# Optimization experiments

Hardware: AMD Instinct MI355X
Metric: run time of the kernel (lower is better)

The kernel has to match this reference:

```python
import jax, jax.numpy as jnp
import numpy as np

GAMMA = 0.9
SCALE_BASE = 512.0


def _xpos(x, downscale=False):
    """XPOS rotary embedding (torchscale variant) applied to x: (B, L, D)."""
    B, L, D = x.shape
    half = D // 2
    # per-channel magnitude base: ((2i) + 0.4*D) / (1.4*D), i over even channels
    scale_vec = (jnp.arange(0, D, 2, dtype=jnp.float32) + 0.4 * D) / (1.4 * D)  # (half,)
    power = jnp.arange(L, dtype=jnp.float32) / SCALE_BASE                        # (L,)
    scale = scale_vec[None, :] ** power[:, None]                                 # (L, half)
    if downscale:
        scale = 1.0 / scale
    # fixed sinusoidal frequencies over `half` dims
    inv_freq = 1.0 / (10000.0 ** (jnp.arange(half, dtype=jnp.float32) / half))   # (half,)
    sinusoid = jnp.arange(L, dtype=jnp.float32)[:, None] * inv_freq[None, :]     # (L, half)
    sin = jnp.repeat(jnp.sin(sinusoid) * scale, 2, axis=-1)                      # (L, D) interleaved dup
    cos = jnp.repeat(jnp.cos(sinusoid) * scale, 2, axis=-1)
    # rotate_every_two: (x0,x1,x2,x3,...) -> (-x1,x0,-x3,x2,...)
    x_even = x[..., 0::2]
    x_odd = x[..., 1::2]
    rot = jnp.stack((-x_odd, x_even), axis=-1).reshape(x.shape)
    return x * cos + rot * sin


def _get_D(seq_len):
    n = jnp.arange(seq_len, dtype=jnp.float32)[:, None]
    m = jnp.arange(seq_len, dtype=jnp.float32)[None, :]
    D = GAMMA ** jnp.abs(n - m)  # non-causal decay, no NaNs since gamma > 0
    return D


def setup_inputs() -> dict:
    key = jax.random.key(0)
    k1, k2, k3, k4 = jax.random.split(key, 4)
    B, L, H, Dh = 8, 2048, 1024, 1024
    X = jax.random.normal(k1, (B, L, H), dtype=jnp.float32)
    W_Q = jax.random.normal(k2, (H, Dh), dtype=jnp.float32) / H
    W_K = jax.random.normal(k3, (H, Dh), dtype=jnp.float32) / H
    W_V = jax.random.normal(k4, (H, Dh), dtype=jnp.float32) / H
    return {"X": X, "W_Q": W_Q, "W_K": W_K, "W_V": W_V}


def reference(X, W_Q, W_K, W_V):
    B, L, H = X.shape
    D = _get_D(L)                       # (L, L)
    Q = _xpos(X @ W_Q)                  # (B, L, Dh)
    K = _xpos(X @ W_K, downscale=True)  # (B, L, Dh)
    V = X @ W_V                         # (B, L, Dv)
    scores = jnp.einsum('bqd,bkd->bqk', Q, K)   # (B, L, L)
    p_attn = jax.nn.softmax(scores, axis=-1)
    p_attn = p_attn * D[None, :, :]              # elementwise decay AFTER softmax
    return jnp.einsum('bqk,bkv->bqv', p_attn, V)
```

## Files before the change

### kernel.cpp

```cpp
#include <hip/hip_runtime.h>
#include <math.h>


#define LDIM 2048
#define HDIM 1024
#define MTOT 16384

typedef unsigned short u16;
typedef unsigned int u32;
typedef __attribute__((ext_vector_type(4))) float f32x4;
typedef __attribute__((ext_vector_type(8))) short s16x8;

#define GLD16(gp, lp) __builtin_amdgcn_global_load_lds( \
    (const __attribute__((address_space(1))) void*)(gp), \
    (__attribute__((address_space(3))) void*)(lp), 16, 0, 0)

__device__ __forceinline__ u16 f2bf(float f) {
    unsigned u = __float_as_uint(f);
    return (u16)((u + 0x7FFFu + ((u >> 16) & 1u)) >> 16);
}

__device__ __forceinline__ void sincos_rev(float ang, float* sn, float* cs) {
    double dr = (double)ang * 0.15915494309189535;
    dr -= __builtin_floor(dr);
    float fr = (float)dr;
    float s_, c_;
    asm("v_sin_f32 %0, %1" : "=v"(s_) : "v"(fr));
    asm("v_cos_f32 %0, %1" : "=v"(c_) : "v"(fr));
    *sn = s_; *cs = c_;
}

__device__ __forceinline__ void gemm256h(const u16* __restrict__ A,
                                         const u16* __restrict__ B,
                                         int lda, int ldb, int K, int m0, int n0,
                                         char* smem, int tid, f32x4 (*acc)[4])
{
    const int wv = tid >> 6, ln = tid & 63;
    const int wm = wv >> 2, wn = wv & 3;
    const int lr = ln & 15, lg = ln >> 4;
    const int srow = tid >> 3;
    const int scol = ((tid & 7) ^ (srow & 7)) * 8;

    const u16* ap[4];
    const u16* bp[4];
#pragma unroll
    for (int r = 0; r < 4; ++r) {
        ap[r] = A + (size_t)(m0 + r * 64 + srow) * lda + scol;
        bp[r] = B + (size_t)(n0 + r * 64 + srow) * ldb + scol;
    }

    int arow[8], brow[4];
#pragma unroll
    for (int fm = 0; fm < 8; ++fm) arow[fm] = (wm * 128 + fm * 16 + lr) * 128;
#pragma unroll
    for (int fn = 0; fn < 4; ++fn) brow[fn] = 32768 + (wn * 64 + fn * 16 + lr) * 128;
    int slotb[2];
#pragma unroll
    for (int kk = 0; kk < 2; ++kk) slotb[kk] = (((kk << 2) | lg) ^ (lr & 7)) << 4;

#define STAGEALL(e_) do { char* d_ = smem + (e_) * 65536 + tid * 16;          \
        _Pragma("unroll") for (int r_ = 0; r_ < 4; ++r_) {                    \
            GLD16(ap[r_], d_ + r_ * 8192);          ap[r_] += 64; }           \
        _Pragma("unroll") for (int r_ = 0; r_ < 4; ++r_) {                    \
            GLD16(bp[r_], d_ + 32768 + r_ * 8192);  bp[r_] += 64; }           \
    } while (0)

#define RD_A(Bb_, mh) do {                                                    \
        _Pragma("unroll") for (int fm_ = 0; fm_ < 4; ++fm_)                   \
            _Pragma("unroll") for (int kk_ = 0; kk_ < 2; ++kk_)               \
                aq[fm_ * 2 + kk_] = *(const s16x8*)((Bb_) +                   \
                    arow[(mh) * 4 + fm_] + slotb[kk_]);                       \
    } while (0)
#define RD_B(Bb_, nh, dst) do {                                               \
        _Pragma("unroll") for (int fn_ = 0; fn_ < 2; ++fn_)                   \
            _Pragma("unroll") for (int kk_ = 0; kk_ < 2; ++kk_)               \
                dst[fn_ * 2 + kk_] = *(const s16x8*)((Bb_) +                  \
                    brow[(nh) * 2 + fn_] + slotb[kk_]);                       \
    } while (0)

#define MFMA16(mh, nh, bq_) do {                                              \
        _Pragma("unroll") for (int fm_ = 0; fm_ < 4; ++fm_)                   \
            _Pragma("unroll") for (int fn_ = 0; fn_ < 2; ++fn_)               \
                _Pragma("unroll") for (int kk_ = 0; kk_ < 2; ++kk_)           \
                    acc[(mh) * 4 + fm_][(nh) * 2 + fn_] =                     \
                        __builtin_amdgcn_mfma_f32_16x16x32_bf16(              \
                            aq[fm_ * 2 + kk_], bq_[fn_ * 2 + kk_],            \
                            acc[(mh) * 4 + fm_][(nh) * 2 + fn_], 0, 0, 0);    \
    } while (0)

    const int nk = K >> 6;

    STAGEALL(0);
    __syncthreads();

    s16x8 aq[8], b0[4], b1[4];

#pragma unroll 1
    for (int t = 0; t < nk; ++t) {
        const int d = t & 1, e = d ^ 1;
        if (t + 1 < nk) STAGEALL(e);
        const char* Bb = smem + d * 65536;
        RD_A(Bb, 0); RD_B(Bb, 0, b0);
        MFMA16(0, 0, b0);
        RD_B(Bb, 1, b1);
        MFMA16(0, 1, b1);
        RD_A(Bb, 1);
        MFMA16(1, 1, b1);
        MFMA16(1, 0, b0);
        __syncthreads();
    }
    __syncthreads();
#undef STAGEALL
#undef RD_A
#undef RD_B
#undef MFMA16
}

__global__ __launch_bounds__(256) void prep_all(
    const float* __restrict__ X,
    const float* __restrict__ Wq, const float* __restrict__ Wk,
    const float* __restrict__ Wv,
    u16* __restrict__ Xb, u16* __restrict__ WT,
    u32* __restrict__ CSq, u32* __restrict__ CSk)
{
    __shared__ float L[64][65];
    const int bid = blockIdx.x;
    if (bid < 2048) {
        const int n4 = MTOT * HDIM / 4;
        int i = bid * 256 + threadIdx.x;
        const int stride = 2048 * 256;
        for (; i < n4; i += stride) {
            float4 v = ((const float4*)X)[i];
            ushort4 o = make_ushort4(f2bf(v.x), f2bf(v.y), f2bf(v.z), f2bf(v.w));
            ((ushort4*)Xb)[i] = o;
        }
    } else if (bid < 4096) {
        const int l = bid - 2048;
        for (int ih = threadIdx.x; ih < 512; ih += 256) {
            float invf = exp2f(-13.287712379549449f * (1.f / 512.f) * (float)ih);
            float sn, cs;
            sincos_rev((float)l * invf, &sn, &cs);
            float l2sv = log2f(((float)(2 * ih) + 409.6f) * (1.f / 1433.6f));
            float e = (float)l * (1.f / 512.f) * l2sv;
            float sq = exp2f(e), sk = exp2f(-e);
            CSq[l * 512 + ih] = (u32)f2bf(cs * sq) | ((u32)f2bf(sn * sq) << 16);
            CSk[l * 512 + ih] = (u32)f2bf(cs * sk) | ((u32)f2bf(sn * sk) << 16);
        }
    } else {
        const int r = bid - 4096;
        const int z = r >> 8;
        const int y = (r >> 4) & 15;
        const int x = r & 15;
        const float* Wz = (z == 0) ? Wq : (z == 1) ? Wk : Wv;
        u16* Oz = WT + (size_t)z * HDIM * HDIM;
        const int k0 = y * 64, n0 = x * 64;
        const int t = threadIdx.x;
        const int r_ = t >> 4, c4 = (t & 15) * 4;
#pragma unroll
        for (int it = 0; it < 4; ++it) {
            const int row = it * 16 + r_;
            float4 v = *(const float4*)&Wz[(size_t)(k0 + row) * HDIM + n0 + c4];
            L[row][c4 + 0] = v.x; L[row][c4 + 1] = v.y;
            L[row][c4 + 2] = v.z; L[row][c4 + 3] = v.w;
        }
        __syncthreads();
#pragma unroll
        for (int it = 0; it < 4; ++it) {
            const int orow = it * 16 + r_;
            ushort4 o = make_ushort4(f2bf(L[c4 + 0][orow]), f2bf(L[c4 + 1][orow]),
                                     f2bf(L[c4 + 2][orow]), f2bf(L[c4 + 3][orow]));
            *(ushort4*)&Oz[(size_t)(n0 + orow) * HDIM + k0 + c4] = o;
        }
    }
}

__global__ __launch_bounds__(512, 2) void qkv_gemm(
    const u16* __restrict__ Xb, const u16* __restrict__ WT,
    const u32* __restrict__ CSq, const u32* __restrict__ CSk,
    u16* __restrict__ Qb, u16* __restrict__ Kb, u16* __restrict__ Vt)
{
    __shared__ __align__(16) char smem[256 * 264 * 2];
    const int bid = blockIdx.x;
    const int xcd = bid & 7, t = bid >> 3;
    const int m8 = t & 7;
    const int n_ = (t >> 3) & 3;
    const int z  = t >> 5;
    const int m0 = (xcd * 8 + m8) * 256;
    const int n0 = n_ * 256;
    const int tid = threadIdx.x;

    f32x4 acc[8][4] = {};

    gemm256h(Xb, WT + (size_t)z * HDIM * HDIM, HDIM, HDIM, HDIM, m0, n0, smem, tid, acc);

    const int wv = tid >> 6, ln = tid & 63;
    const int wm = wv >> 2, wn = wv & 3;
    const int lr = ln & 15, lg = ln >> 4;
    const int l0 = m0 & (LDIM - 1);
    u16* T = (u16*)smem;

    if (z < 2) {
        const u32* CS = (z == 0) ? CSq : CSk;
#pragma unroll
        for (int fn = 0; fn < 4; ++fn) {
            const int gc = n0 + wn * 64 + fn * 16 + lr;
            const int ih = gc >> 1;
            const float sgn = (gc & 1) ? 1.f : -1.f;
            const u32* tb = CS + (size_t)l0 * 512 + ih;
#pragma unroll
            for (int fm = 0; fm < 8; ++fm) {
#pragma unroll
                for (int reg = 0; reg < 4; ++reg) {
                    const int rowl = wm * 128 + fm * 16 + lg * 4 + reg;
                    u32 v = tb[(size_t)rowl * 512];
                    float cs = __uint_as_float(v << 16);
                    float sn = __uint_as_float(v & 0xFFFF0000u);
                    float c = acc[fm][fn][reg];
                    float p = __shfl_xor(c, 1);
                    T[rowl * 264 + wn * 64 + fn * 16 + lr] =
                        f2bf(c * cs + sgn * p * sn);
                }
            }
        }
        __syncthreads();
        u16* Out = (z == 0) ? Qb : Kb;
        const int row_ = tid >> 5, slot = tid & 31;
#pragma unroll
        for (int g = 0; g < 16; ++g) {
            const int row = g * 16 + row_;
            s16x8 v = *(const s16x8*)&T[row * 264 + slot * 8];
            *(s16x8*)&Out[(size_t)(m0 + row) * HDIM + n0 + slot * 8] = v;
        }
    } else {
#pragma unroll
        for (int fn = 0; fn < 4; ++fn)
#pragma unroll
            for (int fm = 0; fm < 8; ++fm) {
                ushort4 o = make_ushort4(f2bf(acc[fm][fn][0]), f2bf(acc[fm][fn][1]),
                                         f2bf(acc[fm][fn][2]), f2bf(acc[fm][fn][3]));
                *(ushort4*)&T[(wn * 64 + fn * 16 + lr) * 264 +
                              wm * 128 + fm * 16 + lg * 4] = o;
            }
        __syncthreads();
        const int b = m0 >> 11;
        const int row_ = tid >> 5, slot = tid & 31;
#pragma unroll
        for (int g = 0; g < 16; ++g) {
            const int row = g * 16 + row_;
            s16x8 v = *(const s16x8*)&T[row * 264 + slot * 8];
            *(s16x8*)&Vt[((size_t)b * HDIM + n0 + row) * LDIM + l0 + slot * 8] = v;
        }
    }
}

__global__ __launch_bounds__(512, 2) void qk_gemm(
    const u16* __restrict__ Q, const u16* __restrict__ Km,
    u16* __restrict__ Wm, float* __restrict__ Zp)
{
    __shared__ __align__(16) char smem[256 * 264 * 2];
    __shared__ float Zl[4][256];
    const int bid = blockIdx.x;
    const int b = bid & 7, t = bid >> 3;
    const int mt = t & 7;
    const int nt = t >> 3;
    const int m0 = mt * 256;
    const int n0 = nt * 256;
    const int tid = threadIdx.x;

    f32x4 acc[8][4] = {};

    gemm256h(Q + (size_t)b * LDIM * HDIM, Km + (size_t)b * LDIM * HDIM,
             HDIM, HDIM, HDIM, m0, n0, smem, tid, acc);

    const int wv = tid >> 6, ln = tid & 63;
    const int wm = wv >> 2, wn = wv & 3;
    const int lr = ln & 15, lg = ln >> 4;
    u16* T = (u16*)smem;
    const float LOG2E = 1.4426950408889634f;
    const float LOG2G = -0.15200309344504997f;

#pragma unroll
    for (int fm = 0; fm < 8; ++fm) {
        float ps[4] = {0.f, 0.f, 0.f, 0.f};
#pragma unroll
        for (int fn = 0; fn < 4; ++fn) {
            const int gk = n0 + wn * 64 + fn * 16 + lr;
#pragma unroll
            for (int reg = 0; reg < 4; ++reg) {
                const int mloc = wm * 128 + fm * 16 + lg * 4 + reg;
                const int gq = m0 + mloc;
                float t1 = acc[fm][fn][reg] * LOG2E;
                float e = exp2f(t1);
                int dd = gq - gk; dd = dd < 0 ? -dd : dd;
                ps[reg] += e;
                T[mloc * 264 + wn * 64 + fn * 16 + lr] =
                    f2bf(exp2f(t1 + (float)dd * LOG2G));
            }
        }
#pragma unroll
        for (int reg = 0; reg < 4; ++reg) {
            float s = ps[reg];
            s += __shfl_xor(s, 1); s += __shfl_xor(s, 2);
            s += __shfl_xor(s, 4); s += __shfl_xor(s, 8);
            if (lr == 0)
                Zl[wn][wm * 128 + fm * 16 + lg * 4 + reg] = s;
        }
    }
    __syncthreads();

    const int row_ = tid >> 5, slot = tid & 31;
#pragma unroll
    for (int g = 0; g < 16; ++g) {
        const int row = g * 16 + row_;
        s16x8 v = *(const s16x8*)&T[row * 264 + slot * 8];
        *(s16x8*)&Wm[((size_t)b * LDIM + m0 + row) * LDIM + n0 + slot * 8] = v;
    }
    if (tid < 256)
        Zp[((size_t)b * 8 + nt) * LDIM + m0 + tid] =
            Zl[0][tid] + Zl[1][tid] + Zl[2][tid] + Zl[3][tid];
}

__global__ __launch_bounds__(512, 2) void pv_gemm(
    const u16* __restrict__ Wm, const u16* __restrict__ Vt,
    const float* __restrict__ Zp, float* __restrict__ Out)
{
    __shared__ __align__(16) char smem[2 * 65536];
    __shared__ float Zinv[256];
    const int bid = blockIdx.x;
    const int b = bid & 7, t = bid >> 3;
    const int mt4 = t & 3;
    const int nt = (t >> 2) & 3;
    const int mtH = t >> 4;
    const int m0 = (mtH * 4 + mt4) * 256;
    const int n0 = nt * 256;
    const int tid = threadIdx.x;

    if (tid < 256) {
        float zz = 0.f;
#pragma unroll
        for (int nb = 0; nb < 8; ++nb)
            zz += Zp[((size_t)b * 8 + nb) * LDIM + m0 + tid];
        Zinv[tid] = 1.0f / zz;
    }
    __syncthreads();

    f32x4 acc[8][4] = {};

    gemm256h(Wm + (size_t)b * LDIM * LDIM, Vt + (size_t)b * HDIM * LDIM,
             LDIM, LDIM, LDIM, m0, n0, smem, tid, acc);

    const int wv = tid >> 6, ln = tid & 63;
    const int wm = wv >> 2, wn = wv & 3;
    const int lr = ln & 15, lg = ln >> 4;
    float* Ob = Out + (size_t)b * LDIM * HDIM;
#pragma unroll
    for (int fm = 0; fm < 8; ++fm)
#pragma unroll
        for (int fn = 0; fn < 4; ++fn) {
            const int gn = n0 + wn * 64 + fn * 16 + lr;
#pragma unroll
            for (int reg = 0; reg < 4; ++reg) {
                const int row = wm * 128 + fm * 16 + lg * 4 + reg;
                Ob[(size_t)(m0 + row) * HDIM + gn] = acc[fm][fn][reg] * Zinv[row];
            }
        }
}

extern "C" void kernel_launch(void* const* d_in, const int* in_sizes, int n_in,
                              void* d_out, int out_size, void* d_ws, size_t ws_size,
                              hipStream_t stream)
{
    (void)in_sizes; (void)n_in; (void)out_size; (void)ws_size;
    const float* X  = (const float*)d_in[0];
    const float* Wq = (const float*)d_in[1];
    const float* Wk = (const float*)d_in[2];
    const float* Wv = (const float*)d_in[3];
    char* ws = (char*)d_ws;
    const size_t MB = 1024 * 1024;

    u16* Wmat = (u16*)ws;
    u16* Xb   = (u16*)ws;
    u16* WT   = (u16*)(ws + 32 * MB);
    u16* Qb   = (u16*)(ws + 64 * MB);
    u16* Kb   = (u16*)(ws + 96 * MB);
    u16* Vt   = (u16*)(ws + 128 * MB);
    float* Zp = (float*)(ws + 160 * MB);
    u32* CSq  = (u32*)(ws + 161 * MB);
    u32* CSk  = (u32*)(ws + 165 * MB);

    prep_all<<<4864, 256, 0, stream>>>(X, Wq, Wk, Wv, Xb, WT, CSq, CSk);
    qkv_gemm<<<768, 512, 0, stream>>>(Xb, WT, CSq, CSk, Qb, Kb, Vt);
    qk_gemm<<<512, 512, 0, stream>>>(Qb, Kb, Wmat, Zp);
    pv_gemm<<<256, 512, 0, stream>>>(Wmat, Vt, Zp, (float*)d_out);
}
```

Measured before the change: 289.5 us.

## Load GEMM B operand directly from global into registers, stage only A in LDS

The shared GEMM core stops staging the B tile through LDS. Each wave now loads its own B fragments straight from global memory into registers, double-buffered in two register sets, and only A goes through LDS. This halves LDS traffic and footprint (pv_gemm's shared buffer shrinks to 64KB) and removes the B LDS reads. The cost is more VGPRs, uncoalesced per-lane global loads of B replicated across the two wm waves, and a loop that assumes an even K-step count.

```diff
diff --git a/kernel.cpp b/kernel.cpp
--- a/kernel.cpp
+++ b/kernel.cpp
@@ -30,7 +30,7 @@
     *sn = s_; *cs = c_;
 }
 
-__device__ __forceinline__ void gemm256h(const u16* __restrict__ A,
+__device__ __forceinline__ void gemm256r(const u16* __restrict__ A,
                                          const u16* __restrict__ B,
                                          int lda, int ldb, int K, int m0, int n0,
                                          char* smem, int tid, f32x4 (*acc)[4])
@@ -42,27 +42,32 @@
     const int scol = ((tid & 7) ^ (srow & 7)) * 8;
 
     const u16* ap[4];
-    const u16* bp[4];
-#pragma unroll
-    for (int r = 0; r < 4; ++r) {
+#pragma unroll
+    for (int r = 0; r < 4; ++r)
         ap[r] = A + (size_t)(m0 + r * 64 + srow) * lda + scol;
-        bp[r] = B + (size_t)(n0 + r * 64 + srow) * ldb + scol;
-    }
-
-    int arow[8], brow[4];
+
+    const u16* bgp[4];
+#pragma unroll
+    for (int fn = 0; fn < 4; ++fn)
+        bgp[fn] = B + (size_t)(n0 + wn * 64 + fn * 16 + lr) * ldb + lg * 8;
+
+    int arow[8];
 #pragma unroll
     for (int fm = 0; fm < 8; ++fm) arow[fm] = (wm * 128 + fm * 16 + lr) * 128;
-#pragma unroll
-    for (int fn = 0; fn < 4; ++fn) brow[fn] = 32768 + (wn * 64 + fn * 16 + lr) * 128;
     int slotb[2];
 #pragma unroll
     for (int kk = 0; kk < 2; ++kk) slotb[kk] = (((kk << 2) | lg) ^ (lr & 7)) << 4;
 
-#define STAGEALL(e_) do { char* d_ = smem + (e_) * 65536 + tid * 16;          \
+#define STAGEA(e_) do { char* d_ = smem + (e_) * 32768 + tid * 16;            \
         _Pragma("unroll") for (int r_ = 0; r_ < 4; ++r_) {                    \
-            GLD16(ap[r_], d_ + r_ * 8192);          ap[r_] += 64; }           \
-        _Pragma("unroll") for (int r_ = 0; r_ < 4; ++r_) {                    \
-            GLD16(bp[r_], d_ + 32768 + r_ * 8192);  bp[r_] += 64; }           \
+            GLD16(ap[r_], d_ + r_ * 8192); ap[r_] += 64; }                    \
+    } while (0)
+
+#define LOADB(dst) do { _Pragma("unroll")                                     \
+        for (int fn_ = 0; fn_ < 4; ++fn_) {                                   \
+            dst[fn_ * 2 + 0] = *(const s16x8*)(bgp[fn_]);                     \
+            dst[fn_ * 2 + 1] = *(const s16x8*)(bgp[fn_] + 32);                \
+            bgp[fn_] += 64; }                                                 \
     } while (0)
 
 #define RD_A(Bb_, mh) do {                                                    \
@@ -71,48 +76,49 @@
                 aq[fm_ * 2 + kk_] = *(const s16x8*)((Bb_) +                   \
                     arow[(mh) * 4 + fm_] + slotb[kk_]);                       \
     } while (0)
-#define RD_B(Bb_, nh, dst) do {                                               \
-        _Pragma("unroll") for (int fn_ = 0; fn_ < 2; ++fn_)                   \
-            _Pragma("unroll") for (int kk_ = 0; kk_ < 2; ++kk_)               \
-                dst[fn_ * 2 + kk_] = *(const s16x8*)((Bb_) +                  \
-                    brow[(nh) * 2 + fn_] + slotb[kk_]);                       \
-    } while (0)
-
-#define MFMA16(mh, nh, bq_) do {                                              \
+
+#define MFMA16(mh, nh, bq) do {                                               \
         _Pragma("unroll") for (int fm_ = 0; fm_ < 4; ++fm_)                   \
             _Pragma("unroll") for (int fn_ = 0; fn_ < 2; ++fn_)               \
                 _Pragma("unroll") for (int kk_ = 0; kk_ < 2; ++kk_)           \
                     acc[(mh) * 4 + fm_][(nh) * 2 + fn_] =                     \
                         __builtin_amdgcn_mfma_f32_16x16x32_bf16(              \
-                            aq[fm_ * 2 + kk_], bq_[fn_ * 2 + kk_],            \
+                            aq[fm_ * 2 + kk_], bq[((nh) * 2 + fn_) * 2 + kk_],\
                             acc[(mh) * 4 + fm_][(nh) * 2 + fn_], 0, 0, 0);    \
     } while (0)
 
     const int nk = K >> 6;
 
-    STAGEALL(0);
+    s16x8 aq[8], bE[8], bO[8];
+
+    LOADB(bE);
+    STAGEA(0);
     __syncthreads();
 
-    s16x8 aq[8], b0[4], b1[4];
-
 #pragma unroll 1
-    for (int t = 0; t < nk; ++t) {
-        const int d = t & 1, e = d ^ 1;
-        if (t + 1 < nk) STAGEALL(e);
-        const char* Bb = smem + d * 65536;
-        RD_A(Bb, 0); RD_B(Bb, 0, b0);
-        MFMA16(0, 0, b0);
-        RD_B(Bb, 1, b1);
-        MFMA16(0, 1, b1);
-        RD_A(Bb, 1);
-        MFMA16(1, 1, b1);
-        MFMA16(1, 0, b0);
-        __syncthreads();
-    }
-    __syncthreads();
-#undef STAGEALL
+    for (int t = 0; t < nk; t += 2) {
+        {
+            STAGEA(1); LOADB(bO);
+            const char* Bb = smem;
+            RD_A(Bb, 0);
+            MFMA16(0, 0, bE); MFMA16(0, 1, bE);
+            RD_A(Bb, 1);
+            MFMA16(1, 1, bE); MFMA16(1, 0, bE);
+            __syncthreads();
+        }
+        {
+            if (t + 2 < nk) { STAGEA(0); LOADB(bE); }
+            const char* Bb = smem + 32768;
+            RD_A(Bb, 0);
+            MFMA16(0, 0, bO); MFMA16(0, 1, bO);
+            RD_A(Bb, 1);
+            MFMA16(1, 1, bO); MFMA16(1, 0, bO);
+            __syncthreads();
+        }
+    }
+#undef STAGEA
+#undef LOADB
 #undef RD_A
-#undef RD_B
 #undef MFMA16
 }
 
@@ -191,7 +197,7 @@
 
     f32x4 acc[8][4] = {};
 
-    gemm256h(Xb, WT + (size_t)z * HDIM * HDIM, HDIM, HDIM, HDIM, m0, n0, smem, tid, acc);
+    gemm256r(Xb, WT + (size_t)z * HDIM * HDIM, HDIM, HDIM, HDIM, m0, n0, smem, tid, acc);
 
     const int wv = tid >> 6, ln = tid & 63;
     const int wm = wv >> 2, wn = wv & 3;
@@ -269,7 +275,7 @@
 
     f32x4 acc[8][4] = {};
 
-    gemm256h(Q + (size_t)b * LDIM * HDIM, Km + (size_t)b * LDIM * HDIM,
+    gemm256r(Q + (size_t)b * LDIM * HDIM, Km + (size_t)b * LDIM * HDIM,
              HDIM, HDIM, HDIM, m0, n0, smem, tid, acc);
 
     const int wv = tid >> 6, ln = tid & 63;
@@ -324,7 +330,7 @@
     const u16* __restrict__ Wm, const u16* __restrict__ Vt,
     const float* __restrict__ Zp, float* __restrict__ Out)
 {
-    __shared__ __align__(16) char smem[2 * 65536];
+    __shared__ __align__(16) char smem[2 * 32768];
     __shared__ float Zinv[256];
     const int bid = blockIdx.x;
     const int b = bid & 7, t = bid >> 3;
@@ -346,7 +352,7 @@
 
     f32x4 acc[8][4] = {};
 
-    gemm256h(Wm + (size_t)b * LDIM * LDIM, Vt + (size_t)b * HDIM * LDIM,
+    gemm256r(Wm + (size_t)b * LDIM * LDIM, Vt + (size_t)b * HDIM * LDIM,
              LDIM, LDIM, LDIM, m0, n0, smem, tid, acc);
 
     const int wv = tid >> 6, ln = tid & 63;
```

After: 410.6 us. 1.42x slower.
